# Performance work log

Hardware: AMD Instinct MI355X
Metric: run time of the kernel (lower is better)

## Reference

```python
import jax, jax.numpy as jnp
import numpy as np

# region/recall params from layer config
NUM_CLASSES = 20
NUM_ANCHORS = 5
ANCHORS = jnp.array([[1.3221, 1.73145], [3.19275, 4.00944], [5.05587, 8.09892],
                     [9.47112, 4.84053], [11.2364, 10.0071]], dtype=jnp.float32)
CONF_THRESH = 0.5
NMS_THRESH = 0.45
IOU_THRESH = 0.5
EPS = 1e-6


def setup_inputs() -> dict:
    key = jax.random.key(0)
    k1, k2 = jax.random.split(key)
    output = jax.random.normal(k1, (8, NUM_ANCHORS * (5 + NUM_CLASSES), 19, 19), dtype=jnp.float32)
    target = jax.random.uniform(k2, (8, 250), dtype=jnp.float32)  # [B, 50*5] rows: cls,cx,cy,w,h
    return {"output": output, "target": target}


def decode_region_boxes(output):
    """get_region_boxes: anchor decode. output [B, A*(5+C), H, W] -> boxes [B, A*H*W, 4] cxcywh (normalized), det_conf [B, A*H*W]."""
    B, _, H, W = output.shape
    o = output.reshape(B, NUM_ANCHORS, 5 + NUM_CLASSES, H, W)
    gx = jnp.arange(W, dtype=output.dtype)
    gy = jnp.arange(H, dtype=output.dtype)
    cx = (jax.nn.sigmoid(o[:, :, 0]) + gx[None, None, None, :]) / W
    cy = (jax.nn.sigmoid(o[:, :, 1]) + gy[None, None, :, None]) / H
    bw = jnp.exp(o[:, :, 2]) * (ANCHORS[:, 0] / W)[None, :, None, None]
    bh = jnp.exp(o[:, :, 3]) * (ANCHORS[:, 1] / H)[None, :, None, None]
    det_conf = jax.nn.sigmoid(o[:, :, 4])
    boxes = jnp.stack([cx, cy, bw, bh], axis=-1).reshape(B, -1, 4)
    return boxes, det_conf.reshape(B, -1)


def pairwise_iou(a, b):
    """bbox_iou(x1y1x2y2=False) for all pairs. a [..., Na, 4], b [..., Nb, 4] cxcywh -> [..., Na, Nb]."""
    ax1 = (a[..., 0] - a[..., 2] * 0.5)[..., :, None]
    ax2 = (a[..., 0] + a[..., 2] * 0.5)[..., :, None]
    ay1 = (a[..., 1] - a[..., 3] * 0.5)[..., :, None]
    ay2 = (a[..., 1] + a[..., 3] * 0.5)[..., :, None]
    bx1 = (b[..., 0] - b[..., 2] * 0.5)[..., None, :]
    bx2 = (b[..., 0] + b[..., 2] * 0.5)[..., None, :]
    by1 = (b[..., 1] - b[..., 3] * 0.5)[..., None, :]
    by2 = (b[..., 1] + b[..., 3] * 0.5)[..., None, :]
    uw = jnp.maximum(ax2, bx2) - jnp.minimum(ax1, bx1)
    uh = jnp.maximum(ay2, by2) - jnp.minimum(ay1, by1)
    aw = a[..., 2][..., :, None]; ah = a[..., 3][..., :, None]
    bw = b[..., 2][..., None, :]; bh = b[..., 3][..., None, :]
    cw = aw + bw - uw
    ch = ah + bh - uh
    carea = jnp.where((cw > 0) & (ch > 0), cw * ch, 0.0)
    uarea = aw * ah + bw * bh - carea
    return carea / uarea


def greedy_nms_keep(iou_mat, valid):
    """Sequential greedy NMS over conf-sorted boxes using precomputed IoU. iou_mat [N,N], valid [N] bool."""
    N = valid.shape[0]
    idx = jnp.arange(N)
    def body(i, keep):
        sup = keep[i] & (iou_mat[i] > NMS_THRESH) & (idx > i)
        return keep & (~sup)
    return jax.lax.fori_loop(0, N, body, valid)


def reference(output, target):
    B = output.shape[0]
    boxes, det = decode_region_boxes(output)              # [B,N,4], [B,N]
    # sort by det_conf descending (nms sort order)
    order = jnp.argsort(-det, axis=1)
    boxes = jnp.take_along_axis(boxes, order[..., None], axis=1)
    det = jnp.take_along_axis(det, order, axis=1)
    valid = det > CONF_THRESH                             # boxes that enter nms (conf filter in get_region_boxes)
    iou_mat = pairwise_iou(boxes, boxes)                  # [B,N,N]
    keep = jax.vmap(greedy_nms_keep)(iou_mat, valid)      # [B,N]
    proposals = jnp.sum(keep)
    # ground truth: [B,T,5] rows [cls,cx,cy,w,h]; num_gts = boxes until first cx==0
    truths = target.reshape(B, -1, 5)
    gt_valid = jnp.cumprod((truths[..., 1] != 0).astype(jnp.int32), axis=1).astype(bool)  # [B,T]
    total = jnp.sum(gt_valid)
    iou_gt = pairwise_iou(truths[..., 1:5], boxes)        # [B,T,N]
    best_iou = jnp.max(jnp.where(keep[:, None, :], iou_gt, 0.0), axis=-1)  # [B,T]
    correct = jnp.sum(gt_valid & (best_iou > IOU_THRESH))
    total_f = total.astype(jnp.float32)
    prop_f = proposals.astype(jnp.float32)
    corr_f = correct.astype(jnp.float32)
    precision = corr_f / (prop_f + EPS)
    recall = corr_f / (total_f + EPS)
    fscore = 2.0 * precision * recall / (precision + recall + EPS)
    return jnp.stack([total_f, prop_f, corr_f, precision, recall, fscore])
```

## Files before the change

kernel.cpp:

```cpp
#include <hip/hip_runtime.h>

namespace {
constexpr int NA    = 5;
constexpr int NCELL = 361;
constexpr int NBOX  = 1805;
constexpr int SORTN = 2048;
constexpr int NT1   = 256;
constexpr int TMAX  = 50;
constexpr float CONF_T = 0.5f;
constexpr float NMS_T  = 0.45f;
constexpr float IOU_T  = 0.5f;
constexpr int NWMAX   = 32;
constexpr int ROWPAD  = 1856;
constexpr int SOA_STRIDE = ROWPAD;
constexpr int SOA_ARR    = 8 * SOA_STRIDE;
constexpr size_t WS_COUNT = 0;
constexpr size_t WS_M     = 64;
constexpr size_t WS_SOA   = 256;
constexpr size_t WS_SUP   = 360448;
}

__device__ __constant__ float d_anchw[NA] = {1.3221f, 3.19275f, 5.05587f, 9.47112f, 11.2364f};
__device__ __constant__ float d_anchh[NA] = {1.73145f, 4.00944f, 8.09892f, 4.84053f, 10.0071f};

__device__ inline unsigned long long shflx64(unsigned long long v, int m) {
    int lo = __shfl_xor((int)(unsigned)(v & 0xffffffffull), m, 64);
    int hi = __shfl_xor((int)(unsigned)(v >> 32), m, 64);
    return ((unsigned long long)(unsigned)hi << 32) | (unsigned)lo;
}
__device__ inline unsigned long long rdlane64(unsigned long long v, int l) {
    unsigned lo = (unsigned)__builtin_amdgcn_readlane((int)(unsigned)(v & 0xffffffffull), l);
    unsigned hi = (unsigned)__builtin_amdgcn_readlane((int)(unsigned)(v >> 32), l);
    return ((unsigned long long)hi << 32) | lo;
}

__global__ __launch_bounds__(NT1, 1) void k_decode_sort(
    const float* __restrict__ net, float* __restrict__ soa,
    int* __restrict__ Marr, int* __restrict__ counters)
{
    __shared__ unsigned long long skey[SORTN];
    __shared__ float4 sbox[NBOX];
    __shared__ int sM;
    const int b = blockIdx.x, tid = threadIdx.x;
    const float* op = net + (size_t)b * (NA * 25 * NCELL);
    if (tid == 0) sM = 0;
    if (b == 0 && tid < 4) counters[tid] = 0;

    for (int n = tid; n < NBOX; n += NT1) {
        int a = n / NCELL;
        int r = n - a * NCELL;
        int y = r / 19;
        int x = r - y * 19;
        int base = a * 25 * NCELL + r;
        float t0 = op[base];
        float t1 = op[base + 1 * NCELL];
        float t2 = op[base + 2 * NCELL];
        float t3 = op[base + 3 * NCELL];
        float t4 = op[base + 4 * NCELL];
        float cx = (1.0f / (1.0f + expf(-t0)) + (float)x) / 19.0f;
        float cy = (1.0f / (1.0f + expf(-t1)) + (float)y) / 19.0f;
        float bw = expf(t2) * (d_anchw[a] / 19.0f);
        float bh = expf(t3) * (d_anchh[a] / 19.0f);
        float det = 1.0f / (1.0f + expf(-t4));
        sbox[n] = make_float4(cx, cy, bw, bh);
        skey[n] = ((unsigned long long)(~__float_as_uint(det)) << 32) | (unsigned)n;
    }
    for (int n = NBOX + tid; n < SORTN; n += NT1) skey[n] = ~0ull;
    __syncthreads();

    unsigned long long v[8];
    const int base8 = tid << 3;
    auto cas = [&](int x, int y, bool up) {
        unsigned long long a = v[x], c = v[y];
        if ((a > c) == up) { v[x] = c; v[y] = a; }
    };
    {
        #pragma unroll
        for (int p = 0; p < 8; ++p) v[p] = skey[base8 + p];
        cas(0,1,true); cas(2,3,false); cas(4,5,true); cas(6,7,false);
        cas(0,2,true); cas(1,3,true); cas(4,6,false); cas(5,7,false);
        cas(0,1,true); cas(2,3,true); cas(4,5,false); cas(6,7,false);
        bool u8 = ((base8 & 8) == 0);
        cas(0,4,u8); cas(1,5,u8); cas(2,6,u8); cas(3,7,u8);
        cas(0,2,u8); cas(1,3,u8); cas(4,6,u8); cas(5,7,u8);
        cas(0,1,u8); cas(2,3,u8); cas(4,5,u8); cas(6,7,u8);
        #pragma unroll
        for (int p = 0; p < 8; ++p) skey[base8 + p] = v[p];
    }
    __syncthreads();
    for (unsigned k = 16; k <= SORTN; k <<= 1) {
        for (unsigned j = k >> 1; j >= 8; j >>= 1) {
            #pragma unroll
            for (int c = 0; c < 4; ++c) {
                unsigned m = (tid << 2) + c;
                unsigned i = ((m & ~(j - 1)) << 1) | (m & (j - 1));
                unsigned p = i | j;
                bool up = ((i & k) == 0);
                unsigned long long a = skey[i], c2 = skey[p];
                if ((a > c2) == up) { skey[i] = c2; skey[p] = a; }
            }
            __syncthreads();
        }
        {
            #pragma unroll
            for (int p = 0; p < 8; ++p) v[p] = skey[base8 + p];
            bool up = ((base8 & k) == 0);
            cas(0,4,up); cas(1,5,up); cas(2,6,up); cas(3,7,up);
            cas(0,2,up); cas(1,3,up); cas(4,6,up); cas(5,7,up);
            cas(0,1,up); cas(2,3,up); cas(4,5,up); cas(6,7,up);
            #pragma unroll
            for (int p = 0; p < 8; ++p) skey[base8 + p] = v[p];
        }
        __syncthreads();
    }

    float* X1 = soa + 0 * SOA_ARR + b * SOA_STRIDE;
    float* Y1 = soa + 1 * SOA_ARR + b * SOA_STRIDE;
    float* X2 = soa + 2 * SOA_ARR + b * SOA_STRIDE;
    float* Y2 = soa + 3 * SOA_ARR + b * SOA_STRIDE;
    float* Wd = soa + 4 * SOA_ARR + b * SOA_STRIDE;
    float* Hd = soa + 5 * SOA_ARR + b * SOA_STRIDE;
    for (int p = tid; p < NBOX; p += NT1) {
        unsigned long long kk = skey[p];
        int n = (int)(unsigned)(kk & 0xffffffffull);
        float det = __uint_as_float(~(unsigned)(kk >> 32));
        float4 bx = sbox[n];
        X1[p] = bx.x - 0.5f * bx.z;
        Y1[p] = bx.y - 0.5f * bx.w;
        X2[p] = bx.x + 0.5f * bx.z;
        Y2[p] = bx.y + 0.5f * bx.w;
        Wd[p] = bx.z;
        Hd[p] = bx.w;
        if (det > CONF_T) {
            float dn = 0.0f;
            if (p + 1 < NBOX) dn = __uint_as_float(~(unsigned)(skey[p + 1] >> 32));
            if (!(dn > CONF_T)) sM = p + 1;
        }
    }
    __syncthreads();
    if (tid == 0) Marr[b] = sM;
}

__global__ __launch_bounds__(256) void k_iou_maskT(
    const float* __restrict__ soa, const int* __restrict__ Marr,
    unsigned long long* __restrict__ supT)
{
    const int blk  = blockIdx.x;
    const int b    = blk & 7;
    const int lane = threadIdx.x & 63;
    const int i    = (blk >> 3) * 4 + (threadIdx.x >> 6);
    const int M = Marr[b];
    if (i >= M) return;
    const float* X1 = soa + 0 * SOA_ARR + b * SOA_STRIDE;
    const float* Y1 = soa + 1 * SOA_ARR + b * SOA_STRIDE;
    const float* X2 = soa + 2 * SOA_ARR + b * SOA_STRIDE;
    const float* Y2 = soa + 3 * SOA_ARR + b * SOA_STRIDE;
    const float* Wd = soa + 4 * SOA_ARR + b * SOA_STRIDE;
    const float* Hd = soa + 5 * SOA_ARR + b * SOA_STRIDE;
    float ax1 = X1[i], ay1 = Y1[i], ax2 = X2[i], ay2 = Y2[i];
    float aw = Wd[i], ah = Hd[i], aarea = aw * ah;
    const int nch = (M + 63) >> 6;
    unsigned long long myw = 0;
    for (int w = 0; w < nch; ++w) {
        int j = (w << 6) + lane;
        bool pred = false;
        if (j > i && j < M) {
            float bw = Wd[j], bh = Hd[j];
            float uw = fmaxf(ax2, X2[j]) - fminf(ax1, X1[j]);
            float uh = fmaxf(ay2, Y2[j]) - fminf(ay1, Y1[j]);
            float cw = aw + bw - uw;
            float ch = ah + bh - uh;
            if (cw > 0.0f && ch > 0.0f) {
                float ca = cw * ch;
                float ua = aarea + bw * bh - ca;
                pred = ca > NMS_T * ua;
            }
        }
        unsigned long long m = __ballot(pred);
        if (w == lane) myw = m;
    }
    if (lane < nch)
        supT[((size_t)b * 32 + lane) * ROWPAD + i] = myw;
}

__global__ __launch_bounds__(1024, 1) void k_sweep(
    const float* __restrict__ soa, const float* __restrict__ tgt,
    const int* __restrict__ Marr, const unsigned long long* __restrict__ supT,
    int* __restrict__ counters, float* __restrict__ out)
{
    __shared__ float X1s[NBOX], Y1s[NBOX], X2s[NBOX], Y2s[NBOX];
    __shared__ float Wss[NBOX], Hss[NBOX];
    __shared__ unsigned long long rmw[NWMAX], keepw[NWMAX];
    __shared__ int sNV, sCorr, sProp;
    const int b = blockIdx.x, tid = threadIdx.x;
    const int wv = tid >> 6, lane = tid & 63;
    const int M = Marr[b];
    const int nwa = (M + 63) >> 6;
    const unsigned long long* sb = supT + (size_t)b * 32 * ROWPAD;

    if (tid < NWMAX) { rmw[tid] = 0ull; keepw[tid] = 0ull; }
    if (tid == 0) { sCorr = 0; sProp = 0; }

    {
        const float* X1 = soa + 0 * SOA_ARR + b * SOA_STRIDE;
        const float* Y1 = soa + 1 * SOA_ARR + b * SOA_STRIDE;
        const float* X2 = soa + 2 * SOA_ARR + b * SOA_STRIDE;
        const float* Y2 = soa + 3 * SOA_ARR + b * SOA_STRIDE;
        const float* Wd = soa + 4 * SOA_ARR + b * SOA_STRIDE;
        const float* Hd = soa + 5 * SOA_ARR + b * SOA_STRIDE;
        for (int p = tid; p < NBOX; p += 1024) {
            X1s[p] = X1[p]; Y1s[p] = Y1[p];
            X2s[p] = X2[p]; Y2s[p] = Y2[p];
            Wss[p] = Wd[p]; Hss[p] = Hd[p];
        }
    }
    if (wv == 2) {
        float cxv = (lane < TMAX) ? tgt[b * 250 + lane * 5 + 1] : 0.0f;
        unsigned long long bm = __ballot(cxv != 0.0f);
        unsigned long long inv = (~bm) & ((1ull << TMAX) - 1);
        if (lane == 0) sNV = inv ? (__ffsll((long long)inv) - 1) : TMAX;
    }

    const int w1 = (wv >= 1) ? wv : -1;
    const int w2 = (wv >= 1 && wv + 15 <= 28) ? (wv + 15) : -1;
    unsigned long long cur1 = 0, cur2 = 0, diag = 0;
    if (wv == 0 && nwa > 0) diag = sb[lane];
    if (w1 >= 1 && w1 < nwa) cur1 = sb[(size_t)w1 * ROWPAD + lane];
    if (w2 >= 1 && w2 < nwa) cur2 = sb[(size_t)w2 * ROWPAD + lane];
    __syncthreads();

    for (int t = 0; t < nwa; ++t) {
        if (wv == 0) {
            unsigned long long cur = rmw[t];
            int rem = M - (t << 6);
            unsigned long long vm = (rem >= 64) ? ~0ull : ((1ull << rem) - 1ull);
            unsigned long long live = vm & ~cur;
            while (live) {
                int i = __ffsll((long long)live) - 1;
                unsigned long long w64 = rdlane64(diag, i);
                cur |= w64;
                live &= ~w64;
                live &= ~(1ull << i);
            }
            unsigned long long kp = vm & ~cur;
            if (lane == 0) keepw[t] = kp;
            int tn = t + 1;
            if (tn < nwa) diag = sb[(size_t)tn * ROWPAD + (tn << 6) + lane];
        }
        __syncthreads();
        {
            unsigned long long kmt = keepw[t];
            if (w1 > t && w1 < nwa) {
                unsigned long long c = ((kmt >> lane) & 1ull) ? cur1 : 0ull;
                c |= shflx64(c, 1);  c |= shflx64(c, 2);  c |= shflx64(c, 4);
                c |= shflx64(c, 8);  c |= shflx64(c, 16); c |= shflx64(c, 32);
                if (lane == 0) rmw[w1] |= c;
            }
            if (w2 > t && w2 < nwa) {
                unsigned long long c = ((kmt >> lane) & 1ull) ? cur2 : 0ull;
                c |= shflx64(c, 1);  c |= shflx64(c, 2);  c |= shflx64(c, 4);
                c |= shflx64(c, 8);  c |= shflx64(c, 16); c |= shflx64(c, 32);
                if (lane == 0) rmw[w2] |= c;
            }
            if (w1 > t + 1 && w1 < nwa) cur1 = sb[(size_t)w1 * ROWPAD + ((t + 1) << 6) + lane];
            if (w2 > t + 1 && w2 < nwa) cur2 = sb[(size_t)w2 * ROWPAD + ((t + 1) << 6) + lane];
        }
        __syncthreads();
    }

    if (wv == 0) {
        unsigned long long kv = (lane < NWMAX) ? keepw[lane] : 0ull;
        int pc = __popcll(kv);
        for (int d = 32; d > 0; d >>= 1) pc += __shfl_down(pc, d, 64);
        if (lane == 0) sProp = pc;
    }

    const int nv = sNV;
    for (int t = wv; t < nv; t += 16) {
        const float* g = tgt + b * 250 + t * 5;
        float gcx = g[1], gcy = g[2], gw = g[3], gh = g[4];
        float gx1 = gcx - 0.5f * gw, gx2 = gcx + 0.5f * gw;
        float gy1 = gcy - 0.5f * gh, gy2 = gcy + 0.5f * gh;
        float garea = gw * gh;
        float best = 0.0f;
        for (int j0 = 0; j0 < M; j0 += 64) {
            int j = j0 + lane;
            bool ok = (j < M) && ((keepw[j0 >> 6] >> lane) & 1ull);
            int js = (j < NBOX) ? j : (NBOX - 1);
            float bw = Wss[js], bh = Hss[js];
            float uw = fmaxf(gx2, X2s[js]) - fminf(gx1, X1s[js]);
            float uh = fmaxf(gy2, Y2s[js]) - fminf(gy1, Y1s[js]);
            float cww = gw + bw - uw, chh = gh + bh - uh;
            float ca = (cww > 0.0f && chh > 0.0f) ? cww * chh : 0.0f;
            float ua = garea + bw * bh - ca;
            float iou = ca / ua;
            best = fmaxf(best, ok ? iou : 0.0f);
        }
        for (int d = 32; d > 0; d >>= 1) best = fmaxf(best, __shfl_down(best, d, 64));
        if (lane == 0 && best > IOU_T) atomicAdd(&sCorr, 1);
    }
    __syncthreads();

    if (tid == 0) {
        atomicAdd(counters + 0, sProp);
        atomicAdd(counters + 1, sCorr);
        atomicAdd(counters + 2, sNV);
        __threadfence();
        int done = atomicAdd(counters + 3, 1);
        if (done == 7) {
            float prop  = (float)atomicAdd(counters + 0, 0);
            float corr  = (float)atomicAdd(counters + 1, 0);
            float total = (float)atomicAdd(counters + 2, 0);
            float prec = corr / (prop + 1e-6f);
            float rec  = corr / (total + 1e-6f);
            float fs   = 2.0f * prec * rec / (prec + rec + 1e-6f);
            out[0] = total;
            out[1] = prop;
            out[2] = corr;
            out[3] = prec;
            out[4] = rec;
            out[5] = fs;
        }
    }
}

extern "C" void kernel_launch(void* const* d_in, const int* in_sizes, int n_in,
                              void* d_out, int out_size, void* d_ws, size_t ws_size,
                              hipStream_t stream) {
    const float* net = (const float*)d_in[0];
    const float* tgt = (const float*)d_in[1];
    char* ws = (char*)d_ws;
    int* counters = (int*)(ws + WS_COUNT);
    int* Marr     = (int*)(ws + WS_M);
    float* soa    = (float*)(ws + WS_SOA);
    unsigned long long* supT = (unsigned long long*)(ws + WS_SUP);

    k_decode_sort<<<8, NT1, 0, stream>>>(net, soa, Marr, counters);
    int rowblocks = (NBOX + 3) / 4;
    k_iou_maskT<<<rowblocks * 8, 256, 0, stream>>>(soa, Marr, supT);
    k_sweep<<<8, 1024, 0, stream>>>(soa, tgt, Marr, supT, counters, (float*)d_out);
}
```

Baseline: 141.3 us.

## Use column-oriented suppression mask and single-wave NMS sweep without block barriers

```diff
diff --git a/kernel.cpp b/kernel.cpp
--- a/kernel.cpp
+++ b/kernel.cpp
@@ -10,6 +10,7 @@
 constexpr float CONF_T = 0.5f;
 constexpr float NMS_T  = 0.45f;
 constexpr float IOU_T  = 0.5f;
+constexpr int NW      = 29;
 constexpr int NWMAX   = 32;
 constexpr int ROWPAD  = 1856;
 constexpr int SOA_STRIDE = ROWPAD;
@@ -23,11 +24,6 @@
 __device__ __constant__ float d_anchw[NA] = {1.3221f, 3.19275f, 5.05587f, 9.47112f, 11.2364f};
 __device__ __constant__ float d_anchh[NA] = {1.73145f, 4.00944f, 8.09892f, 4.84053f, 10.0071f};
 
-__device__ inline unsigned long long shflx64(unsigned long long v, int m) {
-    int lo = __shfl_xor((int)(unsigned)(v & 0xffffffffull), m, 64);
-    int hi = __shfl_xor((int)(unsigned)(v >> 32), m, 64);
-    return ((unsigned long long)(unsigned)hi << 32) | (unsigned)lo;
-}
 __device__ inline unsigned long long rdlane64(unsigned long long v, int l) {
     unsigned lo = (unsigned)__builtin_amdgcn_readlane((int)(unsigned)(v & 0xffffffffull), l);
     unsigned hi = (unsigned)__builtin_amdgcn_readlane((int)(unsigned)(v >> 32), l);
@@ -141,64 +137,62 @@
     if (tid == 0) Marr[b] = sM;
 }
 
-__global__ __launch_bounds__(256) void k_iou_maskT(
+__global__ __launch_bounds__(256) void k_iou_colT(
     const float* __restrict__ soa, const int* __restrict__ Marr,
-    unsigned long long* __restrict__ supT)
+    unsigned long long* __restrict__ supC)
 {
     const int blk  = blockIdx.x;
     const int b    = blk & 7;
     const int lane = threadIdx.x & 63;
-    const int i    = (blk >> 3) * 4 + (threadIdx.x >> 6);
+    const int j    = (blk >> 3) * 4 + (threadIdx.x >> 6);
     const int M = Marr[b];
-    if (i >= M) return;
+    if (j >= M) return;
     const float* X1 = soa + 0 * SOA_ARR + b * SOA_STRIDE;
     const float* Y1 = soa + 1 * SOA_ARR + b * SOA_STRIDE;
     const float* X2 = soa + 2 * SOA_ARR + b * SOA_STRIDE;
     const float* Y2 = soa + 3 * SOA_ARR + b * SOA_STRIDE;
     const float* Wd = soa + 4 * SOA_ARR + b * SOA_STRIDE;
     const float* Hd = soa + 5 * SOA_ARR + b * SOA_STRIDE;
-    float ax1 = X1[i], ay1 = Y1[i], ax2 = X2[i], ay2 = Y2[i];
-    float aw = Wd[i], ah = Hd[i], aarea = aw * ah;
-    const int nch = (M + 63) >> 6;
-    unsigned long long myw = 0;
-    for (int w = 0; w < nch; ++w) {
-        int j = (w << 6) + lane;
+    const float bx1 = X1[j], by1 = Y1[j], bx2 = X2[j], by2 = Y2[j];
+    const float bw = Wd[j], bh = Hd[j], barea = bw * bh;
+    const int jw = j >> 6;
+    unsigned long long* outp = supC + (size_t)b * 32 * ROWPAD + j;
+    for (int t = 0; t <= jw; ++t) {
+        int i = (t << 6) + lane;
+        float ax1 = X1[i], ay1 = Y1[i], ax2 = X2[i], ay2 = Y2[i];
+        float aw = Wd[i], ah = Hd[i];
         bool pred = false;
-        if (j > i && j < M) {
-            float bw = Wd[j], bh = Hd[j];
-            float uw = fmaxf(ax2, X2[j]) - fminf(ax1, X1[j]);
-            float uh = fmaxf(ay2, Y2[j]) - fminf(ay1, Y1[j]);
+        if (i < j) {
+            float uw = fmaxf(ax2, bx2) - fminf(ax1, bx1);
+            float uh = fmaxf(ay2, by2) - fminf(ay1, by1);
             float cw = aw + bw - uw;
             float ch = ah + bh - uh;
             if (cw > 0.0f && ch > 0.0f) {
                 float ca = cw * ch;
-                float ua = aarea + bw * bh - ca;
+                float ua = aw * ah + barea - ca;
                 pred = ca > NMS_T * ua;
             }
         }
         unsigned long long m = __ballot(pred);
-        if (w == lane) myw = m;
-    }
-    if (lane < nch)
-        supT[((size_t)b * 32 + lane) * ROWPAD + i] = myw;
-}
-
-__global__ __launch_bounds__(1024, 1) void k_sweep(
+        if (lane == 0) outp[(size_t)t * ROWPAD] = m;
+    }
+}
+
+__global__ __launch_bounds__(512, 1) void k_sweep(
     const float* __restrict__ soa, const float* __restrict__ tgt,
-    const int* __restrict__ Marr, const unsigned long long* __restrict__ supT,
+    const int* __restrict__ Marr, const unsigned long long* __restrict__ supC,
     int* __restrict__ counters, float* __restrict__ out)
 {
     __shared__ float X1s[NBOX], Y1s[NBOX], X2s[NBOX], Y2s[NBOX];
     __shared__ float Wss[NBOX], Hss[NBOX];
-    __shared__ unsigned long long rmw[NWMAX], keepw[NWMAX];
+    __shared__ unsigned long long keepw[NWMAX];
     __shared__ int sNV, sCorr, sProp;
     const int b = blockIdx.x, tid = threadIdx.x;
     const int wv = tid >> 6, lane = tid & 63;
     const int M = Marr[b];
     const int nwa = (M + 63) >> 6;
-    const unsigned long long* sb = supT + (size_t)b * 32 * ROWPAD;
-
-    if (tid < NWMAX) { rmw[tid] = 0ull; keepw[tid] = 0ull; }
+
+    if (tid < NWMAX) keepw[tid] = 0ull;
     if (tid == 0) { sCorr = 0; sProp = 0; }
 
     {
@@ -208,75 +202,57 @@
         const float* Y2 = soa + 3 * SOA_ARR + b * SOA_STRIDE;
         const float* Wd = soa + 4 * SOA_ARR + b * SOA_STRIDE;
         const float* Hd = soa + 5 * SOA_ARR + b * SOA_STRIDE;
-        for (int p = tid; p < NBOX; p += 1024) {
+        for (int p = tid; p < NBOX; p += 512) {
             X1s[p] = X1[p]; Y1s[p] = Y1[p];
             X2s[p] = X2[p]; Y2s[p] = Y2[p];
             Wss[p] = Wd[p]; Hss[p] = Hd[p];
         }
     }
-    if (wv == 2) {
+    if (wv == 1) {
         float cxv = (lane < TMAX) ? tgt[b * 250 + lane * 5 + 1] : 0.0f;
         unsigned long long bm = __ballot(cxv != 0.0f);
         unsigned long long inv = (~bm) & ((1ull << TMAX) - 1);
         if (lane == 0) sNV = inv ? (__ffsll((long long)inv) - 1) : TMAX;
     }
-
-    const int w1 = (wv >= 1) ? wv : -1;
-    const int w2 = (wv >= 1 && wv + 15 <= 28) ? (wv + 15) : -1;
-    unsigned long long cur1 = 0, cur2 = 0, diag = 0;
-    if (wv == 0 && nwa > 0) diag = sb[lane];
-    if (w1 >= 1 && w1 < nwa) cur1 = sb[(size_t)w1 * ROWPAD + lane];
-    if (w2 >= 1 && w2 < nwa) cur2 = sb[(size_t)w2 * ROWPAD + lane];
-    __syncthreads();
-
-    for (int t = 0; t < nwa; ++t) {
-        if (wv == 0) {
-            unsigned long long cur = rmw[t];
+    __syncthreads();
+
+    if (wv == 0 && nwa > 0) {
+        const unsigned long long* sb = supC + (size_t)b * 32 * ROWPAD;
+        unsigned long long kwv = 0;
+        int pcTot = 0;
+        for (int t = 0; t < nwa; ++t) {
+            unsigned long long cur = 0;
+            #pragma unroll
+            for (int tp = 0; tp < NW; ++tp) {
+                if (tp < t) {
+                    unsigned long long v = sb[(size_t)tp * ROWPAD + (t << 6) + lane];
+                    unsigned long long kw = rdlane64(kwv, tp);
+                    cur |= __ballot((v & kw) != 0ull);
+                }
+            }
+            unsigned long long colw = sb[(size_t)t * ROWPAD + (t << 6) + lane];
             int rem = M - (t << 6);
             unsigned long long vm = (rem >= 64) ? ~0ull : ((1ull << rem) - 1ull);
-            unsigned long long live = vm & ~cur;
+            unsigned long long removed = cur;
+            unsigned long long live = vm & ~removed;
             while (live) {
                 int i = __ffsll((long long)live) - 1;
-                unsigned long long w64 = rdlane64(diag, i);
-                cur |= w64;
-                live &= ~w64;
+                unsigned long long w = __ballot(((colw >> i) & 1ull) != 0ull);
+                removed |= w;
+                live &= ~w;
                 live &= ~(1ull << i);
             }
-            unsigned long long kp = vm & ~cur;
-            if (lane == 0) keepw[t] = kp;
-            int tn = t + 1;
-            if (tn < nwa) diag = sb[(size_t)tn * ROWPAD + (tn << 6) + lane];
-        }
-        __syncthreads();
-        {
-            unsigned long long kmt = keepw[t];
-            if (w1 > t && w1 < nwa) {
-                unsigned long long c = ((kmt >> lane) & 1ull) ? cur1 : 0ull;
-                c |= shflx64(c, 1);  c |= shflx64(c, 2);  c |= shflx64(c, 4);
-                c |= shflx64(c, 8);  c |= shflx64(c, 16); c |= shflx64(c, 32);
-                if (lane == 0) rmw[w1] |= c;
-            }
-            if (w2 > t && w2 < nwa) {
-                unsigned long long c = ((kmt >> lane) & 1ull) ? cur2 : 0ull;
-                c |= shflx64(c, 1);  c |= shflx64(c, 2);  c |= shflx64(c, 4);
-                c |= shflx64(c, 8);  c |= shflx64(c, 16); c |= shflx64(c, 32);
-                if (lane == 0) rmw[w2] |= c;
-            }
-            if (w1 > t + 1 && w1 < nwa) cur1 = sb[(size_t)w1 * ROWPAD + ((t + 1) << 6) + lane];
-            if (w2 > t + 1 && w2 < nwa) cur2 = sb[(size_t)w2 * ROWPAD + ((t + 1) << 6) + lane];
-        }
-        __syncthreads();
-    }
-
-    if (wv == 0) {
-        unsigned long long kv = (lane < NWMAX) ? keepw[lane] : 0ull;
-        int pc = __popcll(kv);
-        for (int d = 32; d > 0; d >>= 1) pc += __shfl_down(pc, d, 64);
-        if (lane == 0) sProp = pc;
-    }
+            unsigned long long kp = vm & ~removed;
+            pcTot += __popcll(kp);
+            kwv = (lane == t) ? kp : kwv;
+        }
+        if (lane < NWMAX) keepw[lane] = (lane < nwa) ? kwv : 0ull;
+        if (lane == 0) sProp = pcTot;
+    }
+    __syncthreads();
 
     const int nv = sNV;
-    for (int t = wv; t < nv; t += 16) {
+    for (int t = wv; t < nv; t += 8) {
         const float* g = tgt + b * 250 + t * 5;
         float gcx = g[1], gcy = g[2], gw = g[3], gh = g[4];
         float gx1 = gcx - 0.5f * gw, gx2 = gcx + 0.5f * gw;
@@ -333,10 +309,10 @@
     int* counters = (int*)(ws + WS_COUNT);
     int* Marr     = (int*)(ws + WS_M);
     float* soa    = (float*)(ws + WS_SOA);
-    unsigned long long* supT = (unsigned long long*)(ws + WS_SUP);
+    unsigned long long* supC = (unsigned long long*)(ws + WS_SUP);
 
     k_decode_sort<<<8, NT1, 0, stream>>>(net, soa, Marr, counters);
-    int rowblocks = (NBOX + 3) / 4;
-    k_iou_maskT<<<rowblocks * 8, 256, 0, stream>>>(soa, Marr, supT);
-    k_sweep<<<8, 1024, 0, stream>>>(soa, tgt, Marr, supT, counters, (float*)d_out);
-}
+    int colblocks = (NBOX + 3) / 4;
+    k_iou_colT<<<colblocks * 8, 256, 0, stream>>>(soa, Marr, supC);
+    k_sweep<<<8, 512, 0, stream>>>(soa, tgt, Marr, supC, counters, (float*)d_out);
+}
```

Measured after the change: 174.2 us. +23.3%, slower.
